# Performance work log

Hardware: AMD Instinct MI355X
Metric: run time of the kernel (lower is better)

## Reference

```python
import jax, jax.numpy as jnp
import numpy as np

D_MODEL = 2048
NUM_EXPERTS = 64
TOP_K = 4
N_TOKENS = 16384


def setup_inputs() -> dict:
    key = jax.random.key(0)
    k_u, k_e = jax.random.split(key)
    u = jax.random.normal(k_u, (N_TOKENS, D_MODEL), dtype=jnp.float32)
    # E initialized like torch.randn(d_model, num_experts) * 0.01
    E = jax.random.normal(k_e, (D_MODEL, NUM_EXPERTS), dtype=jnp.float32) * 0.01
    bias = jnp.zeros((NUM_EXPERTS,), dtype=jnp.float32)
    return {"u": u, "E": E, "bias": bias}


def reference(u, E, bias):
    # logits: [N, num_experts]
    logits = u @ E + bias
    scores = jax.nn.softmax(logits, axis=-1)
    # torch.topk returns values sorted descending; lax.top_k matches
    topk_s, topk_i = jax.lax.top_k(scores, TOP_K)
    aux_loss = jnp.sum(jnp.mean(scores, axis=0) ** 2) * NUM_EXPERTS
    return (topk_i, topk_s, scores, aux_loss)
```

## Files before the change

kernel.cpp:

```cpp
#include <hip/hip_runtime.h>
#include <math.h>

#define N_TOK 16384
#define DM    2048
#define NE    64
#define TOPK  4

#define OFF_TI  0
#define OFF_TS  (N_TOK * TOPK)
#define OFF_SC  (2 * N_TOK * TOPK)
#define OFF_AUX (2 * N_TOK * TOPK + N_TOK * NE)

#define MTPB  64
#define RW    128
#define NRND  (DM / RW)
#define KSTR  136
#define PLN   (MTPB * KSTR)

#define EH_OFF   1024
#define ET_ELEMS ((size_t)NE * DM)
#define WS_NEED  (EH_OFF + 4 * ET_ELEMS)

typedef short s8v __attribute__((ext_vector_type(8)));
typedef float f4v __attribute__((ext_vector_type(4)));

__device__ __forceinline__ unsigned short bf16_rne(float x) {
  unsigned int b = __float_as_uint(x);
  b += 0x7FFFu + ((b >> 16) & 1u);
  return (unsigned short)(b >> 16);
}

__global__ __launch_bounds__(256) void router_prep(
    const float* __restrict__ E, unsigned short* __restrict__ eh,
    unsigned short* __restrict__ el, float* __restrict__ ws)
{
  __shared__ float t[32][65];
  const int tid = threadIdx.x;
  if (blockIdx.x == 0 && tid < 128) ws[tid] = 0.f;
  const int k0  = blockIdx.x * 32;
#pragma unroll
  for (int i = 0; i < 2; ++i) {
    const int fi = i * 256 + tid;
    const int kk = fi >> 4, ee = (fi & 15) * 4;
    const float4 v = *(const float4*)(E + (size_t)(k0 + kk) * NE + ee);
    t[kk][ee] = v.x; t[kk][ee + 1] = v.y; t[kk][ee + 2] = v.z; t[kk][ee + 3] = v.w;
  }
  __syncthreads();
  const int j    = tid >> 6;
  const int lane = tid & 63;
  const int ex   = j * 16 + (lane & 15);
  const int kb   = (lane >> 4) * 8;
  unsigned int hw[4], lw[4];
#pragma unroll
  for (int p = 0; p < 4; ++p) {
    unsigned short h[2], l[2];
#pragma unroll
    for (int q = 0; q < 2; ++q) {
      const float x = t[kb + p * 2 + q][ex];
      h[q] = bf16_rne(x);
      l[q] = bf16_rne(x - __uint_as_float((unsigned)h[q] << 16));
    }
    hw[p] = (unsigned)h[0] | ((unsigned)h[1] << 16);
    lw[p] = (unsigned)l[0] | ((unsigned)l[1] << 16);
  }
  const size_t o = (size_t)blockIdx.x * 2048 + j * 512 + lane * 8;
  *(uint4*)(eh + o) = make_uint4(hw[0], hw[1], hw[2], hw[3]);
  *(uint4*)(el + o) = make_uint4(lw[0], lw[1], lw[2], lw[3]);
}

#define LOAD_U(pf, r) do { _Pragma("unroll") \
  for (int i_ = 0; i_ < 8; ++i_) \
    pf[i_] = *(const float4*)(ugp + (size_t)(r) * RW + i_ * 16); } while (0)

#define WRITE_U(pf, base) do { _Pragma("unroll") \
  for (int i_ = 0; i_ < 8; ++i_) { \
    const float4 v_ = pf[i_]; \
    const unsigned short h0_ = bf16_rne(v_.x), h1_ = bf16_rne(v_.y), \
                         h2_ = bf16_rne(v_.z), h3_ = bf16_rne(v_.w); \
    const unsigned short l0_ = bf16_rne(v_.x - __uint_as_float((unsigned)h0_ << 16)); \
    const unsigned short l1_ = bf16_rne(v_.y - __uint_as_float((unsigned)h1_ << 16)); \
    const unsigned short l2_ = bf16_rne(v_.z - __uint_as_float((unsigned)h2_ << 16)); \
    const unsigned short l3_ = bf16_rne(v_.w - __uint_as_float((unsigned)h3_ << 16)); \
    *(uint2*)&sh[(base) + uoff + i_ * 16] = \
      make_uint2((unsigned)h0_ | ((unsigned)h1_ << 16), (unsigned)h2_ | ((unsigned)h3_ << 16)); \
    *(uint2*)&sh[(base) + PLN + uoff + i_ * 16] = \
      make_uint2((unsigned)l0_ | ((unsigned)l1_ << 16), (unsigned)l2_ | ((unsigned)l3_ << 16)); \
  } } while (0)

#define COMPUTE(r, base) do { \
    const int    pk_ = (r) * 4 + kq; \
    const size_t pb_ = (size_t)pk_ * 2048 + lane * 8; \
    s8v ah_[4], al_[4]; \
    _Pragma("unroll") for (int tt_ = 0; tt_ < 4; ++tt_) { \
      ah_[tt_] = *(const s8v*)&sh[(base) + a_off + tt_ * (16 * KSTR)]; \
      al_[tt_] = *(const s8v*)&sh[(base) + PLN + a_off + tt_ * (16 * KSTR)]; \
    } \
    _Pragma("unroll") for (int j_ = 0; j_ < 4; ++j_) { \
      const s8v bh_ = *(const s8v*)&eh[pb_ + j_ * 512]; \
      const s8v bl_ = *(const s8v*)&el[pb_ + j_ * 512]; \
      _Pragma("unroll") for (int tt_ = 0; tt_ < 4; ++tt_) { \
        acc[tt_][j_] = __builtin_amdgcn_mfma_f32_16x16x32_bf16(ah_[tt_], bh_, acc[tt_][j_], 0, 0, 0); \
        acc[tt_][j_] = __builtin_amdgcn_mfma_f32_16x16x32_bf16(ah_[tt_], bl_, acc[tt_][j_], 0, 0, 0); \
        acc[tt_][j_] = __builtin_amdgcn_mfma_f32_16x16x32_bf16(al_[tt_], bh_, acc[tt_][j_], 0, 0, 0); \
        acc[tt_][j_] = __builtin_amdgcn_mfma_f32_16x16x32_bf16(al_[tt_], bl_, acc[tt_][j_], 0, 0, 0); \
      } } } while (0)

__global__ __launch_bounds__(256, 1) void router_main_mfma(
    const float* __restrict__ u, const unsigned short* __restrict__ eh,
    const unsigned short* __restrict__ el, const float* __restrict__ bias,
    float* __restrict__ out, float* __restrict__ ws)
{
  __shared__ __align__(16) unsigned short sh[4 * PLN];

  const int tid  = threadIdx.x;
  const int lane = tid & 63;
  const int kq   = __builtin_amdgcn_readfirstlane(tid >> 6);
  const int lm   = lane & 15;
  const int lk   = lane >> 4;
  const int tok0 = blockIdx.x * MTPB;

  const int srow = tid >> 2, sseg = tid & 3;
  const float* ugp = u + (size_t)(tok0 + srow) * DM + sseg * 4;
  const int uoff = srow * KSTR + sseg * 4;

  const int a_off = lm * KSTR + kq * 32 + lk * 8;

  f4v acc[4][4];
#pragma unroll
  for (int t = 0; t < 4; ++t)
#pragma unroll
    for (int j = 0; j < 4; ++j) acc[t][j] = (f4v){0.f, 0.f, 0.f, 0.f};

  float4 pfA[8], pfB[8];
  LOAD_U(pfA, 0);
  LOAD_U(pfB, 1);
  WRITE_U(pfA, 0);
  __syncthreads();

  for (int rr = 0; rr < NRND; rr += 2) {
    WRITE_U(pfB, 2 * PLN);
    if (rr + 2 < NRND) LOAD_U(pfA, rr + 2);
    COMPUTE(rr, 0);
    __syncthreads();
    if (rr + 2 < NRND) WRITE_U(pfA, 0);
    if (rr + 3 < NRND) LOAD_U(pfB, rr + 3);
    COMPUTE(rr + 1, 2 * PLN);
    __syncthreads();
  }

  float* fin = (float*)sh;
  if (kq < 2) {
#pragma unroll
    for (int t = 0; t < 4; ++t)
#pragma unroll
      for (int j = 0; j < 4; ++j)
#pragma unroll
        for (int q = 0; q < 4; ++q)
          fin[kq * (64 * 68) + (t * 16 + lk * 4 + q) * 68 + j * 16 + lm] = acc[t][j][q];
  }
  __syncthreads();
  if (kq >= 2) {
#pragma unroll
    for (int t = 0; t < 4; ++t)
#pragma unroll
      for (int j = 0; j < 4; ++j)
#pragma unroll
        for (int q = 0; q < 4; ++q)
          fin[(kq - 2) * (64 * 68) + (t * 16 + lk * 4 + q) * 68 + j * 16 + lm] += acc[t][j][q];
  }
  __syncthreads();

  const float be = bias[lane];
  float asum = 0.f;
  for (int tt = 0; tt < 16; ++tt) {
    const int t = kq * 16 + tt;
    float x = fin[t * 68 + lane] + fin[64 * 68 + t * 68 + lane] + be;

    float m = x;
#pragma unroll
    for (int off = 32; off > 0; off >>= 1) m = fmaxf(m, __shfl_xor(m, off));
    float p = expf(x - m);
    float s = p;
#pragma unroll
    for (int off = 32; off > 0; off >>= 1) s += __shfl_xor(s, off);
    float sc = p / s;

    out[OFF_SC + (size_t)(tok0 + t) * NE + lane] = sc;
    asum += sc;

    float v = sc;
#pragma unroll
    for (int k = 0; k < TOPK; ++k) {
      float bv = v;
      int   bi = lane;
#pragma unroll
      for (int off = 32; off > 0; off >>= 1) {
        float ov = __shfl_xor(bv, off);
        int   oi = __shfl_xor(bi, off);
        if (ov > bv || (ov == bv && oi < bi)) { bv = ov; bi = oi; }
      }
      if (lane == k) {
        out[OFF_TI + (size_t)(tok0 + t) * TOPK + k] = (float)bi;
        out[OFF_TS + (size_t)(tok0 + t) * TOPK + k] = bv;
      }
      if (lane == bi) v = -INFINITY;
    }
  }
  atomicAdd(&ws[lane], asum);

  __threadfence();
  __syncthreads();
  unsigned* flg = (unsigned*)sh;
  if (tid == 0) {
    const unsigned t = atomicAdd((unsigned*)&ws[NE], 1u);
    flg[9216] = (t == (unsigned)(gridDim.x - 1)) ? 1u : 0u;
  }
  __syncthreads();
  if (flg[9216] && tid < 64) {
    const float mv = atomicAdd(&ws[tid], 0.f) * (1.0f / N_TOK);
    float v = mv * mv;
#pragma unroll
    for (int off = 32; off > 0; off >>= 1) v += __shfl_xor(v, off);
    if (tid == 0) out[OFF_AUX] = v * (float)NE;
  }
}

#define TPB     64
#define FB_DC   32
#define FB_NCH  (1024 / FB_DC)
#define FB_LSTR 68
#define FB_UB   (TPB * FB_LSTR)
#define FB_EOFF (2 * FB_UB)
#define FB_EB   (2 * FB_DC * NE)

__global__ __launch_bounds__(1024, 4) void router_main_fb(
    const float* __restrict__ u, const float* __restrict__ E,
    const float* __restrict__ bias, float* __restrict__ out,
    float* __restrict__ ws)
{
  __shared__ float smem[FB_EOFF + 2 * FB_EB];

  const int tid  = threadIdx.x;
  const int lane = tid & 63;
  const int wid  = __builtin_amdgcn_readfirstlane(tid >> 6);
  const int eg   = wid & 7;
  const int kh   = wid >> 3;
  const int tok0 = blockIdx.x * TPB;

  const int stok  = tid >> 4;
  const int sdseg = tid & 15;
  const int skh   = sdseg >> 3;
  const int sdsub = (sdseg & 7) * 4;
  const float* sgbase = u + (size_t)(tok0 + stok) * DM + skh * 1024 + sdsub;
  float* swp = smem + stok * FB_LSTR + sdseg * 4;

  const int eq  = tid & 511;
  const int ekh = tid >> 9;
  const float* egbase = E + (size_t)ekh * 1024 * NE + eq * 4;
  float* ewp = smem + FB_EOFF + ekh * (FB_DC * NE) + eq * 4;

  float acc[8];
#pragma unroll
  for (int j = 0; j < 8; ++j) acc[j] = 0.f;

  float4 pf[3];
  pf[0] = *(const float4*)(sgbase + 0 * FB_DC);
  pf[1] = *(const float4*)(sgbase + 1 * FB_DC);
  pf[2] = *(const float4*)(sgbase + 2 * FB_DC);
  float4 epf = *(const float4*)(egbase + 0 * (FB_DC * NE));
  *(float4*)(swp + 0) = pf[0];
  *(float4*)(ewp + 0) = epf;
  epf = *(const float4*)(egbase + 1 * (FB_DC * NE));
  __syncthreads();

  for (int c = 0; c < FB_NCH; ++c) {
    if (c + 1 < FB_NCH) {
      *(float4*)(swp + ((c + 1) & 1) * FB_UB) = pf[(c + 1) % 3];
      *(float4*)(ewp + ((c + 1) & 1) * FB_EB) = epf;
    }
    if (c + 2 < FB_NCH)
      epf = *(const float4*)(egbase + (c + 2) * (FB_DC * NE));
    if (c + 3 < FB_NCH)
      pf[c % 3] = *(const float4*)(sgbase + (c + 3) * FB_DC);

    const float* sb = smem + (c & 1) * FB_UB + lane * FB_LSTR + kh * FB_DC;
    const float* eb = smem + FB_EOFF + (c & 1) * FB_EB + kh * (FB_DC * NE) + eg * 8;
#pragma unroll
    for (int s = 0; s < 8; ++s) {
      float4 uf = *(const float4*)(sb + s * 4);
#pragma unroll
      for (int dd = 0; dd < 4; ++dd) {
        const float* er = eb + (s * 4 + dd) * NE;
        float4 e0 = *(const float4*)(er);
        float4 e1 = *(const float4*)(er + 4);
        const float uv = (&uf.x)[dd];
        acc[0] = fmaf(e0.x, uv, acc[0]);
        acc[1] = fmaf(e0.y, uv, acc[1]);
        acc[2] = fmaf(e0.z, uv, acc[2]);
        acc[3] = fmaf(e0.w, uv, acc[3]);
        acc[4] = fmaf(e1.x, uv, acc[4]);
        acc[5] = fmaf(e1.y, uv, acc[5]);
        acc[6] = fmaf(e1.z, uv, acc[6]);
        acc[7] = fmaf(e1.w, uv, acc[7]);
      }
    }
    __syncthreads();
  }

  float* fin = smem;
  if (kh == 0) {
#pragma unroll
    for (int j = 0; j < 8; ++j) fin[lane * 65 + eg * 8 + j] = acc[j];
  }
  __syncthreads();
  if (kh == 1) {
#pragma unroll
    for (int j = 0; j < 8; ++j) fin[lane * 65 + eg * 8 + j] += acc[j];
  }
  __syncthreads();

  const float be = bias[lane];
  float asum = 0.f;
#pragma unroll
  for (int tt = 0; tt < 4; ++tt) {
    const int t = wid * 4 + tt;
    float x = fin[t * 65 + lane] + be;

    float m = x;
#pragma unroll
    for (int off = 32; off > 0; off >>= 1) m = fmaxf(m, __shfl_xor(m, off));
    float p = expf(x - m);
    float s = p;
#pragma unroll
    for (int off = 32; off > 0; off >>= 1) s += __shfl_xor(s, off);
    float sc = p / s;

    out[OFF_SC + (size_t)(tok0 + t) * NE + lane] = sc;
    asum += sc;

    float v = sc;
#pragma unroll
    for (int k = 0; k < TOPK; ++k) {
      float bv = v;
      int   bi = lane;
#pragma unroll
      for (int off = 32; off > 0; off >>= 1) {
        float ov = __shfl_xor(bv, off);
        int   oi = __shfl_xor(bi, off);
        if (ov > bv || (ov == bv && oi < bi)) { bv = ov; bi = oi; }
      }
      if (lane == k) {
        out[OFF_TI + (size_t)(tok0 + t) * TOPK + k] = (float)bi;
        out[OFF_TS + (size_t)(tok0 + t) * TOPK + k] = bv;
      }
      if (lane == bi) v = -INFINITY;
    }
  }
  atomicAdd(&ws[lane], asum);
}

__global__ void router_aux(const float* __restrict__ ws, float* __restrict__ out)
{
  const int lane = threadIdx.x & 63;
  float m = ws[lane] * (1.0f / N_TOK);
  float v = m * m;
#pragma unroll
  for (int off = 32; off > 0; off >>= 1) v += __shfl_xor(v, off);
  if (lane == 0) out[OFF_AUX] = v * (float)NE;
}

extern "C" void kernel_launch(void* const* d_in, const int* in_sizes, int n_in,
                              void* d_out, int out_size, void* d_ws, size_t ws_size,
                              hipStream_t stream) {
  const float* u    = (const float*)d_in[0];
  const float* E    = (const float*)d_in[1];
  const float* bias = (const float*)d_in[2];
  float* out = (float*)d_out;
  float* ws  = (float*)d_ws;

  if (ws_size >= WS_NEED) {
    unsigned short* eh = (unsigned short*)((char*)ws + EH_OFF);
    unsigned short* el = eh + ET_ELEMS;
    router_prep<<<DM / 32, 256, 0, stream>>>(E, eh, el, ws);
    router_main_mfma<<<N_TOK / MTPB, 256, 0, stream>>>(u, eh, el, bias, out, ws);
  } else {
    hipMemsetAsync(ws, 0, NE * sizeof(float), stream);
    router_main_fb<<<N_TOK / TPB, 1024, 0, stream>>>(u, E, bias, out, ws);
    router_aux<<<1, 64, 0, stream>>>(ws, out);
  }
}
```

Before: 273.6 us.

## Stage fp32 activations into LDS via direct global-to-LDS loads, convert at compute

Activation tiles now go straight from global memory into LDS as fp32 via global_load_lds with an XOR swizzle, so they no longer pass through registers for conversion before the store. The bf16 hi/lo split moves to the point where LDS is read for MFMA. The block grows to 512 threads (8 waves), each covering a K slice of a 256-wide round, with single-stage double buffering and a four-way partial-sum reduction. This removes register pressure and conversion from the staging path, but doubles LDS traffic per element, repeats conversion work per wave, and adds reduction overhead.

```diff
diff --git a/kernel.cpp b/kernel.cpp
--- a/kernel.cpp
+++ b/kernel.cpp
@@ -12,10 +12,9 @@
 #define OFF_AUX (2 * N_TOK * TOPK + N_TOK * NE)
 
 #define MTPB  64
-#define RW    128
+#define RW    256
 #define NRND  (DM / RW)
-#define KSTR  136
-#define PLN   (MTPB * KSTR)
+#define PLN_F (MTPB * RW)
 
 #define EH_OFF   1024
 #define ET_ELEMS ((size_t)NE * DM)
@@ -28,6 +27,21 @@
   unsigned int b = __float_as_uint(x);
   b += 0x7FFFu + ((b >> 16) & 1u);
   return (unsigned short)(b >> 16);
+}
+
+__device__ __forceinline__ void cvt8(float4 a, float4 b, s8v* hi, s8v* lo) {
+  union { s8v v; unsigned u[4]; } H, L;
+  const float f0[4] = {a.x, a.z, b.x, b.z};
+  const float f1[4] = {a.y, a.w, b.y, b.w};
+#pragma unroll
+  for (int i = 0; i < 4; ++i) {
+    const unsigned short h0 = bf16_rne(f0[i]), h1 = bf16_rne(f1[i]);
+    const float l0 = f0[i] - __uint_as_float((unsigned)h0 << 16);
+    const float l1 = f1[i] - __uint_as_float((unsigned)h1 << 16);
+    H.u[i] = (unsigned)h0 | ((unsigned)h1 << 16);
+    L.u[i] = (unsigned)bf16_rne(l0) | ((unsigned)bf16_rne(l1) << 16);
+  }
+  *hi = H.v; *lo = L.v;
 }
 
 __global__ __launch_bounds__(256) void router_prep(
@@ -68,33 +82,26 @@
   *(uint4*)(el + o) = make_uint4(lw[0], lw[1], lw[2], lw[3]);
 }
 
-#define LOAD_U(pf, r) do { _Pragma("unroll") \
-  for (int i_ = 0; i_ < 8; ++i_) \
-    pf[i_] = *(const float4*)(ugp + (size_t)(r) * RW + i_ * 16); } while (0)
-
-#define WRITE_U(pf, base) do { _Pragma("unroll") \
+#define STAGE(buf, r) do { _Pragma("unroll") \
   for (int i_ = 0; i_ < 8; ++i_) { \
-    const float4 v_ = pf[i_]; \
-    const unsigned short h0_ = bf16_rne(v_.x), h1_ = bf16_rne(v_.y), \
-                         h2_ = bf16_rne(v_.z), h3_ = bf16_rne(v_.w); \
-    const unsigned short l0_ = bf16_rne(v_.x - __uint_as_float((unsigned)h0_ << 16)); \
-    const unsigned short l1_ = bf16_rne(v_.y - __uint_as_float((unsigned)h1_ << 16)); \
-    const unsigned short l2_ = bf16_rne(v_.z - __uint_as_float((unsigned)h2_ << 16)); \
-    const unsigned short l3_ = bf16_rne(v_.w - __uint_as_float((unsigned)h3_ << 16)); \
-    *(uint2*)&sh[(base) + uoff + i_ * 16] = \
-      make_uint2((unsigned)h0_ | ((unsigned)h1_ << 16), (unsigned)h2_ | ((unsigned)h3_ << 16)); \
-    *(uint2*)&sh[(base) + PLN + uoff + i_ * 16] = \
-      make_uint2((unsigned)l0_ | ((unsigned)l1_ << 16), (unsigned)l2_ | ((unsigned)l3_ << 16)); \
+    const float* gp_ = ub0 + (size_t)i_ * DM + (size_t)(r) * RW + ((lane ^ i_) << 2); \
+    float* lp_ = shf + (size_t)(buf) * PLN_F + (w * 8 + i_) * RW; \
+    __builtin_amdgcn_global_load_lds( \
+        (const __attribute__((address_space(1))) unsigned int*)gp_, \
+        (__attribute__((address_space(3))) unsigned int*)lp_, 16, 0, 0); \
   } } while (0)
 
-#define COMPUTE(r, base) do { \
-    const int    pk_ = (r) * 4 + kq; \
-    const size_t pb_ = (size_t)pk_ * 2048 + lane * 8; \
+#define COMPUTE(r, buf) do { \
+    const float* bp_ = shf + (size_t)(buf) * PLN_F; \
     s8v ah_[4], al_[4]; \
     _Pragma("unroll") for (int tt_ = 0; tt_ < 4; ++tt_) { \
-      ah_[tt_] = *(const s8v*)&sh[(base) + a_off + tt_ * (16 * KSTR)]; \
-      al_[tt_] = *(const s8v*)&sh[(base) + PLN + a_off + tt_ * (16 * KSTR)]; \
+      const float* rb_ = bp_ + (tt_ * 16 + lm) * RW; \
+      const int ga_ = (w * 8 + lk * 2) ^ (lm & 7); \
+      const float4 fa_ = *(const float4*)(rb_ + ga_ * 4); \
+      const float4 fb_ = *(const float4*)(rb_ + (ga_ ^ 1) * 4); \
+      cvt8(fa_, fb_, &ah_[tt_], &al_[tt_]); \
     } \
+    const size_t pb_ = (size_t)((r) * 8 + w) * 2048 + lane * 8; \
     _Pragma("unroll") for (int j_ = 0; j_ < 4; ++j_) { \
       const s8v bh_ = *(const s8v*)&eh[pb_ + j_ * 512]; \
       const s8v bl_ = *(const s8v*)&el[pb_ + j_ * 512]; \
@@ -105,25 +112,21 @@
         acc[tt_][j_] = __builtin_amdgcn_mfma_f32_16x16x32_bf16(al_[tt_], bl_, acc[tt_][j_], 0, 0, 0); \
       } } } while (0)
 
-__global__ __launch_bounds__(256, 1) void router_main_mfma(
+__global__ __launch_bounds__(512, 1) void router_main_mfma(
     const float* __restrict__ u, const unsigned short* __restrict__ eh,
     const unsigned short* __restrict__ el, const float* __restrict__ bias,
     float* __restrict__ out, float* __restrict__ ws)
 {
-  __shared__ __align__(16) unsigned short sh[4 * PLN];
+  __shared__ __align__(16) float shf[2 * PLN_F];
 
   const int tid  = threadIdx.x;
   const int lane = tid & 63;
-  const int kq   = __builtin_amdgcn_readfirstlane(tid >> 6);
+  const int w    = __builtin_amdgcn_readfirstlane(tid >> 6);
   const int lm   = lane & 15;
   const int lk   = lane >> 4;
   const int tok0 = blockIdx.x * MTPB;
 
-  const int srow = tid >> 2, sseg = tid & 3;
-  const float* ugp = u + (size_t)(tok0 + srow) * DM + sseg * 4;
-  const int uoff = srow * KSTR + sseg * 4;
-
-  const int a_off = lm * KSTR + kq * 32 + lk * 8;
+  const float* ub0 = u + (size_t)(tok0 + w * 8) * DM;
 
   f4v acc[4][4];
 #pragma unroll
@@ -131,50 +134,45 @@
 #pragma unroll
     for (int j = 0; j < 4; ++j) acc[t][j] = (f4v){0.f, 0.f, 0.f, 0.f};
 
-  float4 pfA[8], pfB[8];
-  LOAD_U(pfA, 0);
-  LOAD_U(pfB, 1);
-  WRITE_U(pfA, 0);
-  __syncthreads();
-
-  for (int rr = 0; rr < NRND; rr += 2) {
-    WRITE_U(pfB, 2 * PLN);
-    if (rr + 2 < NRND) LOAD_U(pfA, rr + 2);
-    COMPUTE(rr, 0);
+  STAGE(0, 0);
+  __syncthreads();
+
+  int cur = 0;
+  for (int r = 0; r < NRND; ++r) {
+    if (r + 1 < NRND) STAGE(cur ^ 1, r + 1);
+    COMPUTE(r, cur);
     __syncthreads();
-    if (rr + 2 < NRND) WRITE_U(pfA, 0);
-    if (rr + 3 < NRND) LOAD_U(pfB, rr + 3);
-    COMPUTE(rr + 1, 2 * PLN);
-    __syncthreads();
-  }
-
-  float* fin = (float*)sh;
-  if (kq < 2) {
+    cur ^= 1;
+  }
+
+  float* fin = shf;
+  if (w < 4) {
 #pragma unroll
     for (int t = 0; t < 4; ++t)
 #pragma unroll
       for (int j = 0; j < 4; ++j)
 #pragma unroll
         for (int q = 0; q < 4; ++q)
-          fin[kq * (64 * 68) + (t * 16 + lk * 4 + q) * 68 + j * 16 + lm] = acc[t][j][q];
-  }
-  __syncthreads();
-  if (kq >= 2) {
+          fin[w * (64 * 68) + (t * 16 + lk * 4 + q) * 68 + j * 16 + lm] = acc[t][j][q];
+  }
+  __syncthreads();
+  if (w >= 4) {
 #pragma unroll
     for (int t = 0; t < 4; ++t)
 #pragma unroll
       for (int j = 0; j < 4; ++j)
 #pragma unroll
         for (int q = 0; q < 4; ++q)
-          fin[(kq - 2) * (64 * 68) + (t * 16 + lk * 4 + q) * 68 + j * 16 + lm] += acc[t][j][q];
+          fin[(w - 4) * (64 * 68) + (t * 16 + lk * 4 + q) * 68 + j * 16 + lm] += acc[t][j][q];
   }
   __syncthreads();
 
   const float be = bias[lane];
   float asum = 0.f;
-  for (int tt = 0; tt < 16; ++tt) {
-    const int t = kq * 16 + tt;
-    float x = fin[t * 68 + lane] + fin[64 * 68 + t * 68 + lane] + be;
+  for (int tt = 0; tt < 8; ++tt) {
+    const int t = w * 8 + tt;
+    float x = fin[t * 68 + lane] + fin[4352 + t * 68 + lane]
+            + fin[2 * 4352 + t * 68 + lane] + fin[3 * 4352 + t * 68 + lane] + be;
 
     float m = x;
 #pragma unroll
@@ -210,13 +208,13 @@
 
   __threadfence();
   __syncthreads();
-  unsigned* flg = (unsigned*)sh;
+  unsigned* flg = (unsigned*)shf;
   if (tid == 0) {
     const unsigned t = atomicAdd((unsigned*)&ws[NE], 1u);
-    flg[9216] = (t == (unsigned)(gridDim.x - 1)) ? 1u : 0u;
-  }
-  __syncthreads();
-  if (flg[9216] && tid < 64) {
+    flg[30000] = (t == (unsigned)(gridDim.x - 1)) ? 1u : 0u;
+  }
+  __syncthreads();
+  if (flg[30000] && tid < 64) {
     const float mv = atomicAdd(&ws[tid], 0.f) * (1.0f / N_TOK);
     float v = mv * mv;
 #pragma unroll
@@ -382,7 +380,7 @@
     unsigned short* eh = (unsigned short*)((char*)ws + EH_OFF);
     unsigned short* el = eh + ET_ELEMS;
     router_prep<<<DM / 32, 256, 0, stream>>>(E, eh, el, ws);
-    router_main_mfma<<<N_TOK / MTPB, 256, 0, stream>>>(u, eh, el, bias, out, ws);
+    router_main_mfma<<<N_TOK / MTPB, 512, 0, stream>>>(u, eh, el, bias, out, ws);
   } else {
     hipMemsetAsync(ws, 0, NE * sizeof(float), stream);
     router_main_fb<<<N_TOK / TPB, 1024, 0, stream>>>(u, E, bias, out, ws);
```

New measurement: 287.3 us. 5.0% more time.

## Split router GEMM per-wave by token group and K half, removing block barriers

Applied to the files above, without the earlier changes.

Doubles the block to 8 waves, each owning 16 tokens and one half of the K dimension with its own private LDS staging buffer, so the main loop no longer needs block-wide barriers. The two K halves are reduced through LDS at the end, and the softmax/top-k loop processes 8 tokens per wave. This targets the barrier stalls and aims for more latency hiding. In exchange, each wave reuses E fragments across fewer tokens, so global/L2 traffic for E rises.

```diff
diff --git a/kernel.cpp b/kernel.cpp
--- a/kernel.cpp
+++ b/kernel.cpp
@@ -12,10 +12,11 @@
 #define OFF_AUX (2 * N_TOK * TOPK + N_TOK * NE)
 
 #define MTPB  64
-#define RW    128
-#define NRND  (DM / RW)
-#define KSTR  136
-#define PLN   (MTPB * KSTR)
+#define RW2   128
+#define NR2   8
+#define KS2   136
+#define WPLH  (16 * KS2)
+#define WPL   (2 * WPLH)
 
 #define EH_OFF   1024
 #define ET_ELEMS ((size_t)NE * DM)
@@ -68,11 +69,11 @@
   *(uint4*)(el + o) = make_uint4(lw[0], lw[1], lw[2], lw[3]);
 }
 
-#define LOAD_U(pf, r) do { _Pragma("unroll") \
+#define LOADW(pf, r) do { _Pragma("unroll") \
   for (int i_ = 0; i_ < 8; ++i_) \
-    pf[i_] = *(const float4*)(ugp + (size_t)(r) * RW + i_ * 16); } while (0)
-
-#define WRITE_U(pf, base) do { _Pragma("unroll") \
+    pf[i_] = *(const float4*)(ugw + (size_t)(r) * RW2 + i_ * 16); } while (0)
+
+#define WRITEW(pf) do { _Pragma("unroll") \
   for (int i_ = 0; i_ < 8; ++i_) { \
     const float4 v_ = pf[i_]; \
     const unsigned short h0_ = bf16_rne(v_.x), h1_ = bf16_rne(v_.y), \
@@ -81,100 +82,100 @@
     const unsigned short l1_ = bf16_rne(v_.y - __uint_as_float((unsigned)h1_ << 16)); \
     const unsigned short l2_ = bf16_rne(v_.z - __uint_as_float((unsigned)h2_ << 16)); \
     const unsigned short l3_ = bf16_rne(v_.w - __uint_as_float((unsigned)h3_ << 16)); \
-    *(uint2*)&sh[(base) + uoff + i_ * 16] = \
+    *(uint2*)&shw[uoffw + i_ * 16] = \
       make_uint2((unsigned)h0_ | ((unsigned)h1_ << 16), (unsigned)h2_ | ((unsigned)h3_ << 16)); \
-    *(uint2*)&sh[(base) + PLN + uoff + i_ * 16] = \
+    *(uint2*)&shw[WPLH + uoffw + i_ * 16] = \
       make_uint2((unsigned)l0_ | ((unsigned)l1_ << 16), (unsigned)l2_ | ((unsigned)l3_ << 16)); \
   } } while (0)
 
-#define COMPUTE(r, base) do { \
-    const int    pk_ = (r) * 4 + kq; \
-    const size_t pb_ = (size_t)pk_ * 2048 + lane * 8; \
-    s8v ah_[4], al_[4]; \
-    _Pragma("unroll") for (int tt_ = 0; tt_ < 4; ++tt_) { \
-      ah_[tt_] = *(const s8v*)&sh[(base) + a_off + tt_ * (16 * KSTR)]; \
-      al_[tt_] = *(const s8v*)&sh[(base) + PLN + a_off + tt_ * (16 * KSTR)]; \
-    } \
-    _Pragma("unroll") for (int j_ = 0; j_ < 4; ++j_) { \
-      const s8v bh_ = *(const s8v*)&eh[pb_ + j_ * 512]; \
-      const s8v bl_ = *(const s8v*)&el[pb_ + j_ * 512]; \
-      _Pragma("unroll") for (int tt_ = 0; tt_ < 4; ++tt_) { \
-        acc[tt_][j_] = __builtin_amdgcn_mfma_f32_16x16x32_bf16(ah_[tt_], bh_, acc[tt_][j_], 0, 0, 0); \
-        acc[tt_][j_] = __builtin_amdgcn_mfma_f32_16x16x32_bf16(ah_[tt_], bl_, acc[tt_][j_], 0, 0, 0); \
-        acc[tt_][j_] = __builtin_amdgcn_mfma_f32_16x16x32_bf16(al_[tt_], bh_, acc[tt_][j_], 0, 0, 0); \
-        acc[tt_][j_] = __builtin_amdgcn_mfma_f32_16x16x32_bf16(al_[tt_], bl_, acc[tt_][j_], 0, 0, 0); \
+#define READF(Fh, Fl) do { _Pragma("unroll") \
+  for (int p_ = 0; p_ < 4; ++p_) { \
+    Fh[p_] = *(const s8v*)&shw[a_off + p_ * 32]; \
+    Fl[p_] = *(const s8v*)&shw[WPLH + a_off + p_ * 32]; \
+  } } while (0)
+
+#define COMP(r, Fh, Fl) do { \
+    const size_t pbase_ = ((size_t)(h * 32 + (r) * 4)) * 2048 + lane * 8; \
+    _Pragma("unroll") for (int p_ = 0; p_ < 4; ++p_) { \
+      const size_t pb_ = pbase_ + (size_t)p_ * 2048; \
+      _Pragma("unroll") for (int j_ = 0; j_ < 4; ++j_) { \
+        const s8v bh_ = *(const s8v*)&eh[pb_ + j_ * 512]; \
+        const s8v bl_ = *(const s8v*)&el[pb_ + j_ * 512]; \
+        acc[j_] = __builtin_amdgcn_mfma_f32_16x16x32_bf16(Fh[p_], bh_, acc[j_], 0, 0, 0); \
+        acc[j_] = __builtin_amdgcn_mfma_f32_16x16x32_bf16(Fh[p_], bl_, acc[j_], 0, 0, 0); \
+        acc[j_] = __builtin_amdgcn_mfma_f32_16x16x32_bf16(Fl[p_], bh_, acc[j_], 0, 0, 0); \
+        acc[j_] = __builtin_amdgcn_mfma_f32_16x16x32_bf16(Fl[p_], bl_, acc[j_], 0, 0, 0); \
       } } } while (0)
 
-__global__ __launch_bounds__(256, 1) void router_main_mfma(
+__global__ __launch_bounds__(512, 1) void router_main_mfma(
     const float* __restrict__ u, const unsigned short* __restrict__ eh,
     const unsigned short* __restrict__ el, const float* __restrict__ bias,
     float* __restrict__ out, float* __restrict__ ws)
 {
-  __shared__ __align__(16) unsigned short sh[4 * PLN];
+  __shared__ __align__(16) unsigned short sh[8 * WPL];
 
   const int tid  = threadIdx.x;
   const int lane = tid & 63;
-  const int kq   = __builtin_amdgcn_readfirstlane(tid >> 6);
+  const int wid  = __builtin_amdgcn_readfirstlane(tid >> 6);
+  const int g    = wid & 3;
+  const int h    = wid >> 2;
   const int lm   = lane & 15;
   const int lk   = lane >> 4;
   const int tok0 = blockIdx.x * MTPB;
 
-  const int srow = tid >> 2, sseg = tid & 3;
-  const float* ugp = u + (size_t)(tok0 + srow) * DM + sseg * 4;
-  const int uoff = srow * KSTR + sseg * 4;
-
-  const int a_off = lm * KSTR + kq * 32 + lk * 8;
-
-  f4v acc[4][4];
-#pragma unroll
-  for (int t = 0; t < 4; ++t)
-#pragma unroll
-    for (int j = 0; j < 4; ++j) acc[t][j] = (f4v){0.f, 0.f, 0.f, 0.f};
+  unsigned short* shw = sh + wid * WPL;
+  const float* ugw = u + (size_t)(tok0 + g * 16 + (lane >> 2)) * DM
+                       + h * 1024 + (lane & 3) * 4;
+  const int uoffw = (lane >> 2) * KS2 + (lane & 3) * 4;
+  const int a_off = lm * KS2 + lk * 8;
+
+  f4v acc[4];
+#pragma unroll
+  for (int j = 0; j < 4; ++j) acc[j] = (f4v){0.f, 0.f, 0.f, 0.f};
 
   float4 pfA[8], pfB[8];
-  LOAD_U(pfA, 0);
-  LOAD_U(pfB, 1);
-  WRITE_U(pfA, 0);
-  __syncthreads();
-
-  for (int rr = 0; rr < NRND; rr += 2) {
-    WRITE_U(pfB, 2 * PLN);
-    if (rr + 2 < NRND) LOAD_U(pfA, rr + 2);
-    COMPUTE(rr, 0);
-    __syncthreads();
-    if (rr + 2 < NRND) WRITE_U(pfA, 0);
-    if (rr + 3 < NRND) LOAD_U(pfB, rr + 3);
-    COMPUTE(rr + 1, 2 * PLN);
-    __syncthreads();
-  }
-
+  LOADW(pfA, 0);
+  WRITEW(pfA);
+  LOADW(pfB, 1);
+
+  s8v f0h[4], f0l[4], f1h[4], f1l[4];
+  for (int r = 0; r < NR2; r += 2) {
+    READF(f0h, f0l);
+    if (r + 1 < NR2) WRITEW(pfB);
+    if (r + 2 < NR2) LOADW(pfA, r + 2);
+    COMP(r, f0h, f0l);
+
+    READF(f1h, f1l);
+    if (r + 2 < NR2) WRITEW(pfA);
+    if (r + 3 < NR2) LOADW(pfB, r + 3);
+    COMP(r + 1, f1h, f1l);
+  }
+
+  __syncthreads();
   float* fin = (float*)sh;
-  if (kq < 2) {
-#pragma unroll
-    for (int t = 0; t < 4; ++t)
-#pragma unroll
-      for (int j = 0; j < 4; ++j)
-#pragma unroll
-        for (int q = 0; q < 4; ++q)
-          fin[kq * (64 * 68) + (t * 16 + lk * 4 + q) * 68 + j * 16 + lm] = acc[t][j][q];
-  }
-  __syncthreads();
-  if (kq >= 2) {
-#pragma unroll
-    for (int t = 0; t < 4; ++t)
-#pragma unroll
-      for (int j = 0; j < 4; ++j)
-#pragma unroll
-        for (int q = 0; q < 4; ++q)
-          fin[(kq - 2) * (64 * 68) + (t * 16 + lk * 4 + q) * 68 + j * 16 + lm] += acc[t][j][q];
+  if (h == 0) {
+#pragma unroll
+    for (int j = 0; j < 4; ++j)
+#pragma unroll
+      for (int q = 0; q < 4; ++q)
+        fin[g * (16 * 68) + (lk * 4 + q) * 68 + j * 16 + lm] = acc[j][q];
+  }
+  __syncthreads();
+  if (h == 1) {
+#pragma unroll
+    for (int j = 0; j < 4; ++j)
+#pragma unroll
+      for (int q = 0; q < 4; ++q)
+        fin[g * (16 * 68) + (lk * 4 + q) * 68 + j * 16 + lm] += acc[j][q];
   }
   __syncthreads();
 
   const float be = bias[lane];
   float asum = 0.f;
-  for (int tt = 0; tt < 16; ++tt) {
-    const int t = kq * 16 + tt;
-    float x = fin[t * 68 + lane] + fin[64 * 68 + t * 68 + lane] + be;
+  for (int tt = 0; tt < 8; ++tt) {
+    const int tl = h * 8 + tt;
+    const int t  = g * 16 + tl;
+    float x = fin[g * (16 * 68) + tl * 68 + lane] + be;
 
     float m = x;
 #pragma unroll
@@ -213,10 +214,10 @@
   unsigned* flg = (unsigned*)sh;
   if (tid == 0) {
     const unsigned t = atomicAdd((unsigned*)&ws[NE], 1u);
-    flg[9216] = (t == (unsigned)(gridDim.x - 1)) ? 1u : 0u;
-  }
-  __syncthreads();
-  if (flg[9216] && tid < 64) {
+    flg[17000] = (t == (unsigned)(gridDim.x - 1)) ? 1u : 0u;
+  }
+  __syncthreads();
+  if (flg[17000] && tid < 64) {
     const float mv = atomicAdd(&ws[tid], 0.f) * (1.0f / N_TOK);
     float v = mv * mv;
 #pragma unroll
@@ -382,7 +383,7 @@
     unsigned short* eh = (unsigned short*)((char*)ws + EH_OFF);
     unsigned short* el = eh + ET_ELEMS;
     router_prep<<<DM / 32, 256, 0, stream>>>(E, eh, el, ws);
-    router_main_mfma<<<N_TOK / MTPB, 256, 0, stream>>>(u, eh, el, bias, out, ws);
+    router_main_mfma<<<N_TOK / MTPB, 512, 0, stream>>>(u, eh, el, bias, out, ws);
   } else {
     hipMemsetAsync(ws, 0, NE * sizeof(float), stream);
     router_main_fb<<<N_TOK / TPB, 1024, 0, stream>>>(u, E, bias, out, ws);
```

Result: slower. 322.2 us (+17.8%).
